# Performance work log

Hardware: AMD Instinct MI355X
Metric: run time of the kernel (lower is better)

Reference implementation:

```python
import jax, jax.numpy as jnp
import numpy as np

N = 100000
IN_C = 128
OUT_C = 32
HEADS = 4
E = 1600000
NEG_SLOPE = 0.2


def setup_inputs() -> dict:
    key = jax.random.key(0)
    ks = jax.random.split(key, 8)
    x = jax.random.normal(ks[0], (N, IN_C), dtype=jnp.float32)
    edge_index = jax.random.randint(ks[1], (2, E), 0, N, dtype=jnp.int64)
    # GATConv params (PyG conventions): lin weight [H*C, in], att vectors [H, C], bias [H*C]
    sc = 1.0 / np.sqrt(IN_C)
    W = jax.random.uniform(ks[2], (HEADS * OUT_C, IN_C), dtype=jnp.float32, minval=-sc, maxval=sc)
    att_src = jax.random.normal(ks[3], (HEADS, OUT_C), dtype=jnp.float32) * 0.1
    att_dst = jax.random.normal(ks[4], (HEADS, OUT_C), dtype=jnp.float32) * 0.1
    bias_conv = jnp.zeros((HEADS * OUT_C,), dtype=jnp.float32)
    # final nn.Linear(H*C, C)
    sl = 1.0 / np.sqrt(HEADS * OUT_C)
    W_lin = jax.random.uniform(ks[5], (OUT_C, HEADS * OUT_C), dtype=jnp.float32, minval=-sl, maxval=sl)
    b_lin = jax.random.uniform(ks[6], (OUT_C,), dtype=jnp.float32, minval=-sl, maxval=sl)
    return {"x": x, "edge_index": edge_index, "W": W, "att_src": att_src,
            "att_dst": att_dst, "bias_conv": bias_conv, "W_lin": W_lin, "b_lin": b_lin}


def reference(x, edge_index, W, att_src, att_dst, bias_conv, W_lin, b_lin):
    n = x.shape[0]
    # add self loops (PyG default)
    loops = jnp.arange(n, dtype=edge_index.dtype)
    src = jnp.concatenate([edge_index[0], loops])
    dst = jnp.concatenate([edge_index[1], loops])
    # linear projection, per-head split: [N, H, C]
    h = (x @ W.T).reshape(n, HEADS, OUT_C)
    # per-node attention logits
    a_src = jnp.einsum('nhc,hc->nh', h, att_src)  # [N, H]
    a_dst = jnp.einsum('nhc,hc->nh', h, att_dst)  # [N, H]
    e = a_src[src] + a_dst[dst]                   # [E', H]
    e = jax.nn.leaky_relu(e, NEG_SLOPE)
    # segment softmax over incoming edges per destination node
    m = jax.ops.segment_max(e, dst, num_segments=n)       # [N, H]
    e = jnp.exp(e - m[dst])
    s = jax.ops.segment_sum(e, dst, num_segments=n)       # [N, H]
    alpha = e / s[dst]                                    # [E', H]
    # scatter-aggregate alpha-weighted source features
    msg = alpha[:, :, None] * h[src]                      # [E', H, C]
    out = jax.ops.segment_sum(msg, dst, num_segments=n)   # [N, H, C]
    out = out.reshape(n, HEADS * OUT_C) + bias_conv
    # final linear + ELU
    return jax.nn.elu(out @ W_lin.T + b_lin)
```

## Files before the change

### kernel.cpp

```cpp
#include <hip/hip_runtime.h>
#include <hip/hip_fp16.h>
#include <cstdint>
#include <cstddef>

#define NHEADS 4
#define OUT_C 32
#define HC 128
#define IN_CH 128
#define NEG_SLOPE 0.2f
#define LDSPAD 136
#define KEDGE 4096

typedef _Float16 half8 __attribute__((ext_vector_type(8)));
typedef float floatx4 __attribute__((ext_vector_type(4)));

static inline size_t align256(size_t v) { return (v + 255) & ~(size_t)255; }

__device__ __forceinline__ float lrelu(float v) { return v > 0.f ? v : NEG_SLOPE * v; }

__device__ __forceinline__ float wred_sum(float v) {
    v += __shfl_xor(v, 1);
    v += __shfl_xor(v, 2);
    v += __shfl_xor(v, 4);
    v += __shfl_xor(v, 8);
    v += __shfl_xor(v, 16);
    v += __shfl_xor(v, 32);
    return v;
}

__device__ __forceinline__ unsigned int pack_h2(float a, float b) {
    __half2 h = __floats2half2_rn(a, b);
    return *reinterpret_cast<unsigned int*>(&h);
}
__device__ __forceinline__ float2 unpack_h2(unsigned int u) {
    __half2 h = *reinterpret_cast<__half2*>(&u);
    return __half22float2(h);
}

__global__ void dw(const float* __restrict__ W, _Float16* __restrict__ wh,
                   const int* __restrict__ ei, int* __restrict__ flag) {
    if (blockIdx.x < 64) {
        int idx = blockIdx.x * 256 + threadIdx.x;
        wh[idx] = (_Float16)W[idx];
        return;
    }
    __shared__ int red[256];
    int t = threadIdx.x;
    int acc = 0;
    for (int i = t; i < 1024; i += 256) acc |= ei[2 * i + 1];
    red[t] = acc;
    __syncthreads();
    for (int s = 128; s > 0; s >>= 1) {
        if (t < s) red[t] |= red[t + s];
        __syncthreads();
    }
    if (t == 0) *flag = (red[0] == 0) ? 1 : 0;
}

__global__ __launch_bounds__(256) void gemm_h(const float* __restrict__ x,
                                              const _Float16* __restrict__ wh,
                                              const float* __restrict__ att_src,
                                              const float* __restrict__ att_dst,
                                              __half* __restrict__ h,
                                              float* __restrict__ a_src,
                                              float* __restrict__ a_dst, int n) {
    __shared__ __align__(16) _Float16 Ws[128 * LDSPAD];
    __shared__ __align__(16) _Float16 Xs[128 * LDSPAD];
    int tid = threadIdx.x;
    int rowbase = blockIdx.x << 7;

    const uint4* w4 = (const uint4*)wh;
#pragma unroll
    for (int i = 0; i < 8; ++i) {
        int u = (i << 8) + tid;
        int r = u >> 4, g = u & 15;
        uint4 v = w4[u];
        *(uint4*)&Ws[r * LDSPAD + (g << 3)] = v;
    }
    const float4* x4 = (const float4*)x;
#pragma unroll
    for (int i = 0; i < 16; ++i) {
        int u = (i << 8) + tid;
        int r = u >> 5, c4 = u & 31;
        int row = rowbase + r;
        if (row >= n) row = n - 1;
        float4 v = x4[((size_t)row << 5) + c4];
        uint2 uu;
        uu.x = pack_h2(v.x, v.y);
        uu.y = pack_h2(v.z, v.w);
        *(uint2*)&Xs[r * LDSPAD + (c4 << 2)] = uu;
    }
    __syncthreads();

    int lane = tid & 63, w = tid >> 6;
    int quad = lane >> 4, Lm = lane & 15;
    floatx4 acc[2][8];
#pragma unroll
    for (int rt = 0; rt < 2; ++rt)
#pragma unroll
        for (int c = 0; c < 8; ++c) acc[rt][c] = (floatx4){0.f, 0.f, 0.f, 0.f};

#pragma unroll
    for (int kc = 0; kc < 128; kc += 32) {
        int ko = kc + (quad << 3);
        half8 a0 = *(const half8*)&Xs[((w << 5) + Lm) * LDSPAD + ko];
        half8 a1 = *(const half8*)&Xs[((w << 5) + 16 + Lm) * LDSPAD + ko];
#pragma unroll
        for (int c = 0; c < 8; ++c) {
            half8 b = *(const half8*)&Ws[((c << 4) + Lm) * LDSPAD + ko];
            acc[0][c] = __builtin_amdgcn_mfma_f32_16x16x32_f16(a0, b, acc[0][c], 0, 0, 0);
            acc[1][c] = __builtin_amdgcn_mfma_f32_16x16x32_f16(a1, b, acc[1][c], 0, 0, 0);
        }
    }
    __syncthreads();
#pragma unroll
    for (int rt = 0; rt < 2; ++rt)
#pragma unroll
        for (int c = 0; c < 8; ++c)
#pragma unroll
            for (int i = 0; i < 4; ++i) {
                int rl = (w << 5) + (rt << 4) + (quad << 2) + i;
                int cl = (c << 4) + Lm;
                Xs[rl * LDSPAD + cl] = (_Float16)acc[rt][c][i];
            }
    __syncthreads();
#pragma unroll
    for (int i = 0; i < 8; ++i) {
        int u = (i << 8) + tid;
        int r = u >> 4, g = u & 15;
        int row = rowbase + r;
        if (row < n) {
            uint4 v = *(uint4*)&Xs[r * LDSPAD + (g << 3)];
            *(uint4*)(h + ((size_t)row << 7) + (g << 3)) = v;
        }
    }
    int r = tid >> 1, seg = tid & 1;
    int row = rowbase + r;
    const _Float16* hp = &Xs[r * LDSPAD + (seg << 6)];
    float sa = 0.f, da = 0.f, sb = 0.f, db = 0.f;
#pragma unroll
    for (int g8 = 0; g8 < 8; ++g8) {
        half8 v = *(const half8*)&hp[g8 << 3];
        int co = (seg << 6) + (g8 << 3);
        float4 A1 = *(const float4*)&att_src[co];
        float4 A2 = *(const float4*)&att_src[co + 4];
        float4 D1 = *(const float4*)&att_dst[co];
        float4 D2 = *(const float4*)&att_dst[co + 4];
        float f0 = (float)v[0], f1 = (float)v[1], f2 = (float)v[2], f3 = (float)v[3];
        float f4 = (float)v[4], f5 = (float)v[5], f6 = (float)v[6], f7 = (float)v[7];
        float ts = f0 * A1.x + f1 * A1.y + f2 * A1.z + f3 * A1.w
                 + f4 * A2.x + f5 * A2.y + f6 * A2.z + f7 * A2.w;
        float td = f0 * D1.x + f1 * D1.y + f2 * D1.z + f3 * D1.w
                 + f4 * D2.x + f5 * D2.y + f6 * D2.z + f7 * D2.w;
        if (g8 < 4) { sa += ts; da += td; } else { sb += ts; db += td; }
    }
    if (row < n) {
        int base = (row << 2) + (seg << 1);
        a_src[base] = sa;
        a_src[base + 1] = sb;
        a_dst[base] = da;
        a_dst[base + 1] = db;
    }
}

__global__ void bhist(const int* __restrict__ ei, const int* __restrict__ flag,
                      int* __restrict__ bcount, int E, int sh) {
    __shared__ int c[256];
    int t = threadIdx.x;
    c[t] = 0;
    __syncthreads();
    int f64 = *flag;
    int stride = gridDim.x * 256;
    for (int i = blockIdx.x * 256 + t; i < E; i += stride) {
        int d;
        if (f64) d = (int)((const long long*)ei)[(size_t)E + i];
        else     d = ei[(size_t)E + i];
        atomicAdd(&c[d >> sh], 1);
    }
    __syncthreads();
    if (c[t]) atomicAdd(&bcount[t], c[t]);
}

__global__ void bscan(const int* __restrict__ bcount, int* __restrict__ bucket_base,
                      int* __restrict__ gcursor, int* __restrict__ off,
                      int n, int E, int sh) {
    __shared__ int ts[256];
    int t = threadIdx.x;
    int lo = t << sh, hi = (t + 1) << sh;
    if (hi > n) hi = n;
    int nodes = hi > lo ? hi - lo : 0;
    int v = bcount[t] + nodes;
    ts[t] = v;
    __syncthreads();
    int run = v;
    for (int d = 1; d < 256; d <<= 1) {
        int o = (t >= d) ? ts[t - d] : 0;
        __syncthreads();
        run += o;
        ts[t] = run;
        __syncthreads();
    }
    int excl = run - v;
    bucket_base[t] = excl;
    gcursor[t] = excl;
    if (t == 255) {
        bucket_base[256] = run;
        off[n] = E + n;
    }
}

__global__ __launch_bounds__(256) void bscatter(const int* __restrict__ ei,
                                                const int* __restrict__ flag,
                                                int* __restrict__ gcursor,
                                                int2* __restrict__ bkt,
                                                int E, int n, int sh) {
    __shared__ int cnt[256], base[256], lcur[256];
    int t = threadIdx.x;
    cnt[t] = 0;
    lcur[t] = 0;
    int total = E + n;
    int i0 = blockIdx.x * KEDGE;
    int f64 = *flag;
    int ed[16], es[16];
    __syncthreads();
#pragma unroll
    for (int j = 0; j < 16; ++j) {
        int i = i0 + (j << 8) + t;
        int s = 0, d = -1;
        if (i < total) {
            if (i < E) {
                if (f64) {
                    s = (int)((const long long*)ei)[i];
                    d = (int)((const long long*)ei)[(size_t)E + i];
                } else {
                    s = ei[i];
                    d = ei[(size_t)E + i];
                }
            } else {
                s = d = i - E;
            }
            atomicAdd(&cnt[d >> sh], 1);
        }
        ed[j] = d;
        es[j] = s;
    }
    __syncthreads();
    base[t] = cnt[t] ? atomicAdd(&gcursor[t], cnt[t]) : 0;
    __syncthreads();
#pragma unroll
    for (int j = 0; j < 16; ++j) {
        int d = ed[j];
        if (d >= 0) {
            int b = d >> sh;
            int pos = base[b] + atomicAdd(&lcur[b], 1);
            bkt[pos] = make_int2(d, es[j]);
        }
    }
}

__global__ __launch_bounds__(256) void bsort(const int2* __restrict__ bkt,
                                             const int* __restrict__ bucket_base,
                                             int* __restrict__ off,
                                             int* __restrict__ sorted,
                                             int n, int sh) {
    __shared__ int cnt[512], offl[512], ts[256];
    int t = threadIdx.x, bid = blockIdx.x;
    int node0 = bid << sh;
    int node1 = (bid + 1) << sh;
    if (node1 > n) node1 = n;
    int nn = node1 - node0;
    int e0 = bucket_base[bid], e1 = bucket_base[bid + 1];
    cnt[t] = 0;
    cnt[t + 256] = 0;
    __syncthreads();
    for (int i = e0 + t; i < e1; i += 256) {
        int2 e = bkt[i];
        atomicAdd(&cnt[e.x - node0], 1);
    }
    __syncthreads();
    int a = cnt[t << 1], b = cnt[(t << 1) + 1];
    int s = a + b;
    ts[t] = s;
    __syncthreads();
    int run = s;
    for (int d = 1; d < 256; d <<= 1) {
        int o = (t >= d) ? ts[t - d] : 0;
        __syncthreads();
        run += o;
        ts[t] = run;
        __syncthreads();
    }
    int excl = run - s;
    offl[t << 1] = excl;
    offl[(t << 1) + 1] = excl + a;
    cnt[t << 1] = 0;
    cnt[(t << 1) + 1] = 0;
    __syncthreads();
    for (int i = t; i < nn; i += 256) off[node0 + i] = e0 + offl[i];
    for (int i = e0 + t; i < e1; i += 256) {
        int2 e = bkt[i];
        int li = e.x - node0;
        int pos = e0 + offl[li] + atomicAdd(&cnt[li], 1);
        sorted[pos] = e.y;
    }
}

__device__ __forceinline__ void accum_half(const int* ssrc, const float* sal,
                                           const __half* __restrict__ h,
                                           int deg, int half, int L, int head,
                                           float4& acc) {
    float4 a0 = {0, 0, 0, 0}, a1 = {0, 0, 0, 0}, a2 = {0, 0, 0, 0}, a3 = {0, 0, 0, 0};
    int j = half;
    for (; j + 6 < deg; j += 8) {
        int s0 = ssrc[j], s1 = ssrc[j + 2], s2 = ssrc[j + 4], s3 = ssrc[j + 6];
        float w0 = sal[(j << 2) + head];
        float w1 = sal[((j + 2) << 2) + head];
        float w2 = sal[((j + 4) << 2) + head];
        float w3 = sal[((j + 6) << 2) + head];
        uint2 u0 = *(const uint2*)(h + ((size_t)s0 << 7) + (L << 2));
        uint2 u1 = *(const uint2*)(h + ((size_t)s1 << 7) + (L << 2));
        uint2 u2 = *(const uint2*)(h + ((size_t)s2 << 7) + (L << 2));
        uint2 u3 = *(const uint2*)(h + ((size_t)s3 << 7) + (L << 2));
        float2 f0a = unpack_h2(u0.x), f0b = unpack_h2(u0.y);
        float2 f1a = unpack_h2(u1.x), f1b = unpack_h2(u1.y);
        float2 f2a = unpack_h2(u2.x), f2b = unpack_h2(u2.y);
        float2 f3a = unpack_h2(u3.x), f3b = unpack_h2(u3.y);
        a0.x = fmaf(w0, f0a.x, a0.x); a0.y = fmaf(w0, f0a.y, a0.y);
        a0.z = fmaf(w0, f0b.x, a0.z); a0.w = fmaf(w0, f0b.y, a0.w);
        a1.x = fmaf(w1, f1a.x, a1.x); a1.y = fmaf(w1, f1a.y, a1.y);
        a1.z = fmaf(w1, f1b.x, a1.z); a1.w = fmaf(w1, f1b.y, a1.w);
        a2.x = fmaf(w2, f2a.x, a2.x); a2.y = fmaf(w2, f2a.y, a2.y);
        a2.z = fmaf(w2, f2b.x, a2.z); a2.w = fmaf(w2, f2b.y, a2.w);
        a3.x = fmaf(w3, f3a.x, a3.x); a3.y = fmaf(w3, f3a.y, a3.y);
        a3.z = fmaf(w3, f3b.x, a3.z); a3.w = fmaf(w3, f3b.y, a3.w);
    }
    for (; j < deg; j += 2) {
        int s0 = ssrc[j];
        float w0 = sal[(j << 2) + head];
        uint2 u0 = *(const uint2*)(h + ((size_t)s0 << 7) + (L << 2));
        float2 f0a = unpack_h2(u0.x), f0b = unpack_h2(u0.y);
        a0.x = fmaf(w0, f0a.x, a0.x); a0.y = fmaf(w0, f0a.y, a0.y);
        a0.z = fmaf(w0, f0b.x, a0.z); a0.w = fmaf(w0, f0b.y, a0.w);
    }
    acc.x += a0.x + a1.x + a2.x + a3.x;
    acc.y += a0.y + a1.y + a2.y + a3.y;
    acc.z += a0.z + a1.z + a2.z + a3.z;
    acc.w += a0.w + a1.w + a2.w + a3.w;
}

__global__ __launch_bounds__(256) void aggregate(const __half* __restrict__ h,
                                                 const int* __restrict__ sorted,
                                                 const int* __restrict__ off,
                                                 const float* __restrict__ a_src,
                                                 const float* __restrict__ a_dst,
                                                 const float* __restrict__ bias,
                                                 __half* __restrict__ agg, int n) {
    __shared__ __align__(16) int sh_src[4][64];
    __shared__ __align__(16) float sh_al[4][256];
    int wslot = threadIdx.x >> 6;
    int lane = threadIdx.x & 63;
    int wid = blockIdx.x * 4 + wslot;
    int nw = gridDim.x * 4;
    int L = lane & 31, half = lane >> 5, head = L >> 3;
    float4 b4 = ((const float4*)bias)[L];
    const float4* as4 = (const float4*)a_src;
    const float4* ad4 = (const float4*)a_dst;
    int* ssrc = sh_src[wslot];
    float* sal = sh_al[wslot];

    for (int node = wid; node < n; node += nw) {
        int start = off[node], end = off[node + 1];
        int deg = end - start;
        float4 ad = ad4[node];
        float4 acc = {0.f, 0.f, 0.f, 0.f};
        float4 psum = {0.f, 0.f, 0.f, 0.f};

        if (deg <= 64) {
            bool v = lane < deg;
            int idx = start + (v ? lane : 0);
            int s = sorted[idx];
            float4 as = as4[s];
            float4 p;
            p.x = v ? __expf(lrelu(as.x + ad.x)) : 0.f;
            p.y = v ? __expf(lrelu(as.y + ad.y)) : 0.f;
            p.z = v ? __expf(lrelu(as.z + ad.z)) : 0.f;
            p.w = v ? __expf(lrelu(as.w + ad.w)) : 0.f;
            psum = p;
            ssrc[lane] = s;
            *(float4*)&sal[lane << 2] = p;
            asm volatile("s_waitcnt lgkmcnt(0)" ::: "memory");
            accum_half(ssrc, sal, h, deg, half, L, head, acc);
            asm volatile("" ::: "memory");
        } else {
            for (int bb = 0; bb < deg; bb += 64) {
                int i = bb + lane;
                bool v = i < deg;
                int idx = start + (v ? i : 0);
                int s = sorted[idx];
                float4 as = as4[s];
                float4 p;
                p.x = v ? __expf(lrelu(as.x + ad.x)) : 0.f;
                p.y = v ? __expf(lrelu(as.y + ad.y)) : 0.f;
                p.z = v ? __expf(lrelu(as.z + ad.z)) : 0.f;
                p.w = v ? __expf(lrelu(as.w + ad.w)) : 0.f;
                psum.x += p.x; psum.y += p.y; psum.z += p.z; psum.w += p.w;
                ssrc[lane] = s;
                *(float4*)&sal[lane << 2] = p;
                asm volatile("s_waitcnt lgkmcnt(0)" ::: "memory");
                int cl = deg - bb;
                if (cl > 64) cl = 64;
                accum_half(ssrc, sal, h, cl, half, L, head, acc);
                asm volatile("" ::: "memory");
            }
        }
        float s0 = wred_sum(psum.x), s1 = wred_sum(psum.y);
        float s2 = wred_sum(psum.z), s3 = wred_sum(psum.w);
        float sh = (head == 0) ? s0 : (head == 1) ? s1 : (head == 2) ? s2 : s3;
        float inv = 1.f / sh;
        acc.x += __shfl_xor(acc.x, 32);
        acc.y += __shfl_xor(acc.y, 32);
        acc.z += __shfl_xor(acc.z, 32);
        acc.w += __shfl_xor(acc.w, 32);
        if (lane < 32) {
            float4 res = {fmaf(acc.x, inv, b4.x), fmaf(acc.y, inv, b4.y),
                          fmaf(acc.z, inv, b4.z), fmaf(acc.w, inv, b4.w)};
            uint2 u;
            u.x = pack_h2(res.x, res.y);
            u.y = pack_h2(res.z, res.w);
            *(uint2*)(agg + ((size_t)node << 7) + (L << 2)) = u;
        }
    }
}

__global__ __launch_bounds__(256) void proj(const __half* __restrict__ agg,
                                            const float* __restrict__ W_lin,
                                            const float* __restrict__ b_lin,
                                            float* __restrict__ out, int n) {
    __shared__ float xs[64][132];
    __shared__ float wt[128][36];
    int tid = threadIdx.x;
    const float4* w4 = (const float4*)W_lin;
#pragma unroll
    for (int i = 0; i < 4; ++i) {
        int f4 = (i << 8) + tid;
        int o = f4 >> 5, kk = (f4 & 31) << 2;
        float4 w = w4[f4];
        wt[kk][o] = w.x;
        wt[kk + 1][o] = w.y;
        wt[kk + 2][o] = w.z;
        wt[kk + 3][o] = w.w;
    }
    int rowbase = blockIdx.x << 6;
    const uint4* a4 = (const uint4*)agg;
#pragma unroll
    for (int i = 0; i < 4; ++i) {
        int f8 = (i << 8) + tid;
        int r = f8 >> 4, cc = (f8 & 15) << 3;
        int row = rowbase + r;
        if (row >= n) row = n - 1;
        uint4 u = a4[((size_t)row << 4) + (cc >> 3)];
        float2 f0 = unpack_h2(u.x), f1 = unpack_h2(u.y);
        float2 f2 = unpack_h2(u.z), f3 = unpack_h2(u.w);
        float* xp = &xs[r][cc];
        xp[0] = f0.x; xp[1] = f0.y; xp[2] = f1.x; xp[3] = f1.y;
        xp[4] = f2.x; xp[5] = f2.y; xp[6] = f3.x; xp[7] = f3.y;
    }
    __syncthreads();
    int r = tid >> 2, cg = tid & 3, c0 = cg << 3;
    float acc[8];
#pragma unroll
    for (int j = 0; j < 8; ++j) acc[j] = 0.f;
    for (int k = 0; k < 128; k += 4) {
        float4 xv = *(const float4*)&xs[r][k];
        float xk[4] = {xv.x, xv.y, xv.z, xv.w};
#pragma unroll
        for (int kk = 0; kk < 4; ++kk) {
            float4 wa = *(const float4*)&wt[k + kk][c0];
            float4 wb = *(const float4*)&wt[k + kk][c0 + 4];
            acc[0] = fmaf(xk[kk], wa.x, acc[0]);
            acc[1] = fmaf(xk[kk], wa.y, acc[1]);
            acc[2] = fmaf(xk[kk], wa.z, acc[2]);
            acc[3] = fmaf(xk[kk], wa.w, acc[3]);
            acc[4] = fmaf(xk[kk], wb.x, acc[4]);
            acc[5] = fmaf(xk[kk], wb.y, acc[5]);
            acc[6] = fmaf(xk[kk], wb.z, acc[6]);
            acc[7] = fmaf(xk[kk], wb.w, acc[7]);
        }
    }
    int row = rowbase + r;
    if (row < n) {
        float res[8];
#pragma unroll
        for (int j = 0; j < 8; ++j) {
            float v = acc[j] + b_lin[c0 + j];
            res[j] = v > 0.f ? v : (__expf(v) - 1.f);
        }
        float4* op = (float4*)(out + (size_t)row * 32 + c0);
        op[0] = make_float4(res[0], res[1], res[2], res[3]);
        op[1] = make_float4(res[4], res[5], res[6], res[7]);
    }
}

extern "C" void kernel_launch(void* const* d_in, const int* in_sizes, int n_in,
                              void* d_out, int out_size, void* d_ws, size_t ws_size,
                              hipStream_t stream) {
    const float* x = (const float*)d_in[0];
    const int* ei = (const int*)d_in[1];
    const float* W = (const float*)d_in[2];
    const float* att_src = (const float*)d_in[3];
    const float* att_dst = (const float*)d_in[4];
    const float* bias_conv = (const float*)d_in[5];
    const float* W_lin = (const float*)d_in[6];
    const float* b_lin = (const float*)d_in[7];
    int n = in_sizes[0] / IN_CH;
    int E = in_sizes[1] / 2;

    int sh = 0;
    while (((n + (1 << sh) - 1) >> sh) > 256) sh++;
    int NB = (n + (1 << sh) - 1) >> sh;

    char* ws = (char*)d_ws;
    size_t o = 0;
    auto alloc = [&](size_t bytes) { char* p = ws + o; o = align256(o + bytes); return p; };
    __half* h        = (__half*)alloc((size_t)n * HC * 2);
    __half* agg      = (__half*)alloc((size_t)n * HC * 2);
    _Float16* wh     = (_Float16*)alloc(128 * 128 * 2);
    float* a_src     = (float*)alloc((size_t)n * NHEADS * 4);
    float* a_dst     = (float*)alloc((size_t)n * NHEADS * 4);
    int* off         = (int*)alloc(((size_t)n + 1) * 4);
    int* bcount      = (int*)alloc(256 * 4);
    int* bucket_base = (int*)alloc(257 * 4);
    int* gcursor     = (int*)alloc(256 * 4);
    int* flag        = (int*)alloc(256);
    int* sorted      = (int*)alloc((size_t)(E + n + 64) * 4);
    int2* bkt        = (int2*)alloc((size_t)(E + n + 64) * 8);

    hipMemsetAsync(bcount, 0, 256 * 4, stream);

    dw<<<65, 256, 0, stream>>>(W, wh, ei, flag);
    gemm_h<<<(n + 127) / 128, 256, 0, stream>>>(x, wh, att_src, att_dst, h, a_src, a_dst, n);
    bhist<<<1024, 256, 0, stream>>>(ei, flag, bcount, E, sh);
    bscan<<<1, 256, 0, stream>>>(bcount, bucket_base, gcursor, off, n, E, sh);
    bscatter<<<(E + n + KEDGE - 1) / KEDGE, 256, 0, stream>>>(ei, flag, gcursor, bkt, E, n, sh);
    bsort<<<NB, 256, 0, stream>>>(bkt, bucket_base, off, sorted, n, sh);
    aggregate<<<2048, 256, 0, stream>>>(h, sorted, off, a_src, a_dst, bias_conv, agg, n);
    proj<<<(n + 63) / 64, 256, 0, stream>>>(agg, W_lin, b_lin, (float*)d_out, n);
}
```

Before: 309.6 us.

## Fold small setup kernels into consumers and deepen aggregate gather unroll

Removes the dw and bscan kernels. The fp32-to-fp16 weight conversion moves into gemm_h, the int64 detection is recomputed per block in bhist and bscatter, and the bucket prefix scan is redone redundantly in bscatter and bsort. gcursor now starts at zero, which relies on the memset covering bcount and gcursor together. The aggregate inner loop also gains a 16-edge unrolled stage to keep more gathers in flight. The aim is fewer launches and better memory-level parallelism, at the cost of redundant per-block scans and detection reads, and higher register pressure in aggregate.

```diff
diff --git a/kernel.cpp b/kernel.cpp
--- a/kernel.cpp
+++ b/kernel.cpp
@@ -37,28 +37,26 @@
     return __half22float2(h);
 }
 
-__global__ void dw(const float* __restrict__ W, _Float16* __restrict__ wh,
-                   const int* __restrict__ ei, int* __restrict__ flag) {
-    if (blockIdx.x < 64) {
-        int idx = blockIdx.x * 256 + threadIdx.x;
-        wh[idx] = (_Float16)W[idx];
-        return;
-    }
-    __shared__ int red[256];
+__device__ __forceinline__ int detect_f64(const int* __restrict__ ei, int E, int* sf) {
     int t = threadIdx.x;
+    if (t == 0) *sf = 0;
+    __syncthreads();
+    int lim = E < 1024 ? E : 1024;
     int acc = 0;
-    for (int i = t; i < 1024; i += 256) acc |= ei[2 * i + 1];
-    red[t] = acc;
-    __syncthreads();
-    for (int s = 128; s > 0; s >>= 1) {
-        if (t < s) red[t] |= red[t + s];
-        __syncthreads();
-    }
-    if (t == 0) *flag = (red[0] == 0) ? 1 : 0;
+    for (int i = t; i < lim; i += 256) acc |= ei[2 * i + 1];
+    acc |= __shfl_xor(acc, 1);
+    acc |= __shfl_xor(acc, 2);
+    acc |= __shfl_xor(acc, 4);
+    acc |= __shfl_xor(acc, 8);
+    acc |= __shfl_xor(acc, 16);
+    acc |= __shfl_xor(acc, 32);
+    if ((t & 63) == 0 && acc) atomicOr(sf, 1);
+    __syncthreads();
+    return *sf == 0;
 }
 
 __global__ __launch_bounds__(256) void gemm_h(const float* __restrict__ x,
-                                              const _Float16* __restrict__ wh,
+                                              const float* __restrict__ W,
                                               const float* __restrict__ att_src,
                                               const float* __restrict__ att_dst,
                                               __half* __restrict__ h,
@@ -69,13 +67,16 @@
     int tid = threadIdx.x;
     int rowbase = blockIdx.x << 7;
 
-    const uint4* w4 = (const uint4*)wh;
-#pragma unroll
-    for (int i = 0; i < 8; ++i) {
+    const float4* wf = (const float4*)W;
+#pragma unroll
+    for (int i = 0; i < 16; ++i) {
         int u = (i << 8) + tid;
-        int r = u >> 4, g = u & 15;
-        uint4 v = w4[u];
-        *(uint4*)&Ws[r * LDSPAD + (g << 3)] = v;
+        int r = u >> 5, g = u & 31;
+        float4 v = wf[u];
+        uint2 uu;
+        uu.x = pack_h2(v.x, v.y);
+        uu.y = pack_h2(v.z, v.w);
+        *(uint2*)&Ws[r * LDSPAD + (g << 2)] = uu;
     }
     const float4* x4 = (const float4*)x;
 #pragma unroll
@@ -163,13 +164,13 @@
     }
 }
 
-__global__ void bhist(const int* __restrict__ ei, const int* __restrict__ flag,
-                      int* __restrict__ bcount, int E, int sh) {
+__global__ void bhist(const int* __restrict__ ei, int* __restrict__ bcount,
+                      int E, int sh) {
     __shared__ int c[256];
+    __shared__ int sf;
     int t = threadIdx.x;
     c[t] = 0;
-    __syncthreads();
-    int f64 = *flag;
+    int f64 = detect_f64(ei, E, &sf);
     int stride = gridDim.x * 256;
     for (int i = blockIdx.x * 256 + t; i < E; i += stride) {
         int d;
@@ -181,48 +182,20 @@
     if (c[t]) atomicAdd(&bcount[t], c[t]);
 }
 
-__global__ void bscan(const int* __restrict__ bcount, int* __restrict__ bucket_base,
-                      int* __restrict__ gcursor, int* __restrict__ off,
-                      int n, int E, int sh) {
-    __shared__ int ts[256];
-    int t = threadIdx.x;
-    int lo = t << sh, hi = (t + 1) << sh;
-    if (hi > n) hi = n;
-    int nodes = hi > lo ? hi - lo : 0;
-    int v = bcount[t] + nodes;
-    ts[t] = v;
-    __syncthreads();
-    int run = v;
-    for (int d = 1; d < 256; d <<= 1) {
-        int o = (t >= d) ? ts[t - d] : 0;
-        __syncthreads();
-        run += o;
-        ts[t] = run;
-        __syncthreads();
-    }
-    int excl = run - v;
-    bucket_base[t] = excl;
-    gcursor[t] = excl;
-    if (t == 255) {
-        bucket_base[256] = run;
-        off[n] = E + n;
-    }
-}
-
 __global__ __launch_bounds__(256) void bscatter(const int* __restrict__ ei,
-                                                const int* __restrict__ flag,
+                                                const int* __restrict__ bcount,
                                                 int* __restrict__ gcursor,
                                                 int2* __restrict__ bkt,
                                                 int E, int n, int sh) {
-    __shared__ int cnt[256], base[256], lcur[256];
+    __shared__ int cnt[256], base[256], lcur[256], ts[256];
+    __shared__ int sf;
     int t = threadIdx.x;
     cnt[t] = 0;
     lcur[t] = 0;
+    int f64 = detect_f64(ei, E, &sf);
     int total = E + n;
     int i0 = blockIdx.x * KEDGE;
-    int f64 = *flag;
     int ed[16], es[16];
-    __syncthreads();
 #pragma unroll
     for (int j = 0; j < 16; ++j) {
         int i = i0 + (j << 8) + t;
@@ -244,8 +217,22 @@
         ed[j] = d;
         es[j] = s;
     }
-    __syncthreads();
-    base[t] = cnt[t] ? atomicAdd(&gcursor[t], cnt[t]) : 0;
+    int lo = t << sh, hi = (t + 1) << sh;
+    if (hi > n) hi = n;
+    int nodes = hi > lo ? hi - lo : 0;
+    int v = bcount[t] + nodes;
+    ts[t] = v;
+    __syncthreads();
+    int run = v;
+    for (int d = 1; d < 256; d <<= 1) {
+        int o = (t >= d) ? ts[t - d] : 0;
+        __syncthreads();
+        run += o;
+        ts[t] = run;
+        __syncthreads();
+    }
+    int excl = run - v;
+    base[t] = excl + (cnt[t] ? atomicAdd(&gcursor[t], cnt[t]) : 0);
     __syncthreads();
 #pragma unroll
     for (int j = 0; j < 16; ++j) {
@@ -259,30 +246,19 @@
 }
 
 __global__ __launch_bounds__(256) void bsort(const int2* __restrict__ bkt,
-                                             const int* __restrict__ bucket_base,
+                                             const int* __restrict__ bcount,
                                              int* __restrict__ off,
                                              int* __restrict__ sorted,
-                                             int n, int sh) {
+                                             int n, int E, int sh) {
     __shared__ int cnt[512], offl[512], ts[256];
     int t = threadIdx.x, bid = blockIdx.x;
-    int node0 = bid << sh;
-    int node1 = (bid + 1) << sh;
-    if (node1 > n) node1 = n;
-    int nn = node1 - node0;
-    int e0 = bucket_base[bid], e1 = bucket_base[bid + 1];
-    cnt[t] = 0;
-    cnt[t + 256] = 0;
-    __syncthreads();
-    for (int i = e0 + t; i < e1; i += 256) {
-        int2 e = bkt[i];
-        atomicAdd(&cnt[e.x - node0], 1);
-    }
-    __syncthreads();
-    int a = cnt[t << 1], b = cnt[(t << 1) + 1];
-    int s = a + b;
-    ts[t] = s;
-    __syncthreads();
-    int run = s;
+    int lo = t << sh, hi = (t + 1) << sh;
+    if (hi > n) hi = n;
+    int nodes = hi > lo ? hi - lo : 0;
+    int v = bcount[t] + nodes;
+    ts[t] = v;
+    __syncthreads();
+    int run = v;
     for (int d = 1; d < 256; d <<= 1) {
         int o = (t >= d) ? ts[t - d] : 0;
         __syncthreads();
@@ -290,6 +266,34 @@
         ts[t] = run;
         __syncthreads();
     }
+    int e0 = (bid > 0) ? ts[bid - 1] : 0;
+    int e1 = ts[bid];
+    if (bid == gridDim.x - 1 && t == 0) off[n] = E + n;
+    int node0 = bid << sh;
+    int node1 = (bid + 1) << sh;
+    if (node1 > n) node1 = n;
+    int nn = node1 - node0;
+    __syncthreads();
+    cnt[t] = 0;
+    cnt[t + 256] = 0;
+    __syncthreads();
+    for (int i = e0 + t; i < e1; i += 256) {
+        int2 e = bkt[i];
+        atomicAdd(&cnt[e.x - node0], 1);
+    }
+    __syncthreads();
+    int a = cnt[t << 1], b = cnt[(t << 1) + 1];
+    int s = a + b;
+    ts[t] = s;
+    __syncthreads();
+    run = s;
+    for (int d = 1; d < 256; d <<= 1) {
+        int o = (t >= d) ? ts[t - d] : 0;
+        __syncthreads();
+        run += o;
+        ts[t] = run;
+        __syncthreads();
+    }
     int excl = run - s;
     offl[t << 1] = excl;
     offl[(t << 1) + 1] = excl + a;
@@ -311,6 +315,51 @@
                                            float4& acc) {
     float4 a0 = {0, 0, 0, 0}, a1 = {0, 0, 0, 0}, a2 = {0, 0, 0, 0}, a3 = {0, 0, 0, 0};
     int j = half;
+    for (; j + 14 < deg; j += 16) {
+        int s0 = ssrc[j], s1 = ssrc[j + 2], s2 = ssrc[j + 4], s3 = ssrc[j + 6];
+        int s4 = ssrc[j + 8], s5 = ssrc[j + 10], s6 = ssrc[j + 12], s7 = ssrc[j + 14];
+        float w0 = sal[(j << 2) + head];
+        float w1 = sal[((j + 2) << 2) + head];
+        float w2 = sal[((j + 4) << 2) + head];
+        float w3 = sal[((j + 6) << 2) + head];
+        float w4 = sal[((j + 8) << 2) + head];
+        float w5 = sal[((j + 10) << 2) + head];
+        float w6 = sal[((j + 12) << 2) + head];
+        float w7 = sal[((j + 14) << 2) + head];
+        uint2 u0 = *(const uint2*)(h + ((size_t)s0 << 7) + (L << 2));
+        uint2 u1 = *(const uint2*)(h + ((size_t)s1 << 7) + (L << 2));
+        uint2 u2 = *(const uint2*)(h + ((size_t)s2 << 7) + (L << 2));
+        uint2 u3 = *(const uint2*)(h + ((size_t)s3 << 7) + (L << 2));
+        uint2 u4 = *(const uint2*)(h + ((size_t)s4 << 7) + (L << 2));
+        uint2 u5 = *(const uint2*)(h + ((size_t)s5 << 7) + (L << 2));
+        uint2 u6 = *(const uint2*)(h + ((size_t)s6 << 7) + (L << 2));
+        uint2 u7 = *(const uint2*)(h + ((size_t)s7 << 7) + (L << 2));
+        float2 fa, fb;
+        fa = unpack_h2(u0.x); fb = unpack_h2(u0.y);
+        a0.x = fmaf(w0, fa.x, a0.x); a0.y = fmaf(w0, fa.y, a0.y);
+        a0.z = fmaf(w0, fb.x, a0.z); a0.w = fmaf(w0, fb.y, a0.w);
+        fa = unpack_h2(u1.x); fb = unpack_h2(u1.y);
+        a1.x = fmaf(w1, fa.x, a1.x); a1.y = fmaf(w1, fa.y, a1.y);
+        a1.z = fmaf(w1, fb.x, a1.z); a1.w = fmaf(w1, fb.y, a1.w);
+        fa = unpack_h2(u2.x); fb = unpack_h2(u2.y);
+        a2.x = fmaf(w2, fa.x, a2.x); a2.y = fmaf(w2, fa.y, a2.y);
+        a2.z = fmaf(w2, fb.x, a2.z); a2.w = fmaf(w2, fb.y, a2.w);
+        fa = unpack_h2(u3.x); fb = unpack_h2(u3.y);
+        a3.x = fmaf(w3, fa.x, a3.x); a3.y = fmaf(w3, fa.y, a3.y);
+        a3.z = fmaf(w3, fb.x, a3.z); a3.w = fmaf(w3, fb.y, a3.w);
+        fa = unpack_h2(u4.x); fb = unpack_h2(u4.y);
+        a0.x = fmaf(w4, fa.x, a0.x); a0.y = fmaf(w4, fa.y, a0.y);
+        a0.z = fmaf(w4, fb.x, a0.z); a0.w = fmaf(w4, fb.y, a0.w);
+        fa = unpack_h2(u5.x); fb = unpack_h2(u5.y);
+        a1.x = fmaf(w5, fa.x, a1.x); a1.y = fmaf(w5, fa.y, a1.y);
+        a1.z = fmaf(w5, fb.x, a1.z); a1.w = fmaf(w5, fb.y, a1.w);
+        fa = unpack_h2(u6.x); fb = unpack_h2(u6.y);
+        a2.x = fmaf(w6, fa.x, a2.x); a2.y = fmaf(w6, fa.y, a2.y);
+        a2.z = fmaf(w6, fb.x, a2.z); a2.w = fmaf(w6, fb.y, a2.w);
+        fa = unpack_h2(u7.x); fb = unpack_h2(u7.y);
+        a3.x = fmaf(w7, fa.x, a3.x); a3.y = fmaf(w7, fa.y, a3.y);
+        a3.z = fmaf(w7, fb.x, a3.z); a3.w = fmaf(w7, fb.y, a3.w);
+    }
     for (; j + 6 < deg; j += 8) {
         int s0 = ssrc[j], s1 = ssrc[j + 2], s2 = ssrc[j + 4], s3 = ssrc[j + 6];
         float w0 = sal[(j << 2) + head];
@@ -321,31 +370,32 @@
         uint2 u1 = *(const uint2*)(h + ((size_t)s1 << 7) + (L << 2));
         uint2 u2 = *(const uint2*)(h + ((size_t)s2 << 7) + (L << 2));
         uint2 u3 = *(const uint2*)(h + ((size_t)s3 << 7) + (L << 2));
-        float2 f0a = unpack_h2(u0.x), f0b = unpack_h2(u0.y);
-        float2 f1a = unpack_h2(u1.x), f1b = unpack_h2(u1.y);
-        float2 f2a = unpack_h2(u2.x), f2b = unpack_h2(u2.y);
-        float2 f3a = unpack_h2(u3.x), f3b = unpack_h2(u3.y);
-        a0.x = fmaf(w0, f0a.x, a0.x); a0.y = fmaf(w0, f0a.y, a0.y);
-        a0.z = fmaf(w0, f0b.x, a0.z); a0.w = fmaf(w0, f0b.y, a0.w);
-        a1.x = fmaf(w1, f1a.x, a1.x); a1.y = fmaf(w1, f1a.y, a1.y);
-        a1.z = fmaf(w1, f1b.x, a1.z); a1.w = fmaf(w1, f1b.y, a1.w);
-        a2.x = fmaf(w2, f2a.x, a2.x); a2.y = fmaf(w2, f2a.y, a2.y);
-        a2.z = fmaf(w2, f2b.x, a2.z); a2.w = fmaf(w2, f2b.y, a2.w);
-        a3.x = fmaf(w3, f3a.x, a3.x); a3.y = fmaf(w3, f3a.y, a3.y);
-        a3.z = fmaf(w3, f3b.x, a3.z); a3.w = fmaf(w3, f3b.y, a3.w);
+        float2 fa, fb;
+        fa = unpack_h2(u0.x); fb = unpack_h2(u0.y);
+        a0.x = fmaf(w0, fa.x, a0.x); a0.y = fmaf(w0, fa.y, a0.y);
+        a0.z = fmaf(w0, fb.x, a0.z); a0.w = fmaf(w0, fb.y, a0.w);
+        fa = unpack_h2(u1.x); fb = unpack_h2(u1.y);
+        a1.x = fmaf(w1, fa.x, a1.x); a1.y = fmaf(w1, fa.y, a1.y);
+        a1.z = fmaf(w1, fb.x, a1.z); a1.w = fmaf(w1, fb.y, a1.w);
+        fa = unpack_h2(u2.x); fb = unpack_h2(u2.y);
+        a2.x = fmaf(w2, fa.x, a2.x); a2.y = fmaf(w2, fa.y, a2.y);
+        a2.z = fmaf(w2, fb.x, a2.z); a2.w = fmaf(w2, fb.y, a2.w);
+        fa = unpack_h2(u3.x); fb = unpack_h2(u3.y);
+        a3.x = fmaf(w3, fa.x, a3.x); a3.y = fmaf(w3, fa.y, a3.y);
+        a3.z = fmaf(w3, fb.x, a3.z); a3.w = fmaf(w3, fb.y, a3.w);
     }
     for (; j < deg; j += 2) {
         int s0 = ssrc[j];
         float w0 = sal[(j << 2) + head];
         uint2 u0 = *(const uint2*)(h + ((size_t)s0 << 7) + (L << 2));
-        float2 f0a = unpack_h2(u0.x), f0b = unpack_h2(u0.y);
-        a0.x = fmaf(w0, f0a.x, a0.x); a0.y = fmaf(w0, f0a.y, a0.y);
-        a0.z = fmaf(w0, f0b.x, a0.z); a0.w = fmaf(w0, f0b.y, a0.w);
-    }
-    acc.x += a0.x + a1.x + a2.x + a3.x;
-    acc.y += a0.y + a1.y + a2.y + a3.y;
-    acc.z += a0.z + a1.z + a2.z + a3.z;
-    acc.w += a0.w + a1.w + a2.w + a3.w;
+        float2 fa = unpack_h2(u0.x), fb = unpack_h2(u0.y);
+        a0.x = fmaf(w0, fa.x, a0.x); a0.y = fmaf(w0, fa.y, a0.y);
+        a0.z = fmaf(w0, fb.x, a0.z); a0.w = fmaf(w0, fb.y, a0.w);
+    }
+    acc.x += (a0.x + a1.x) + (a2.x + a3.x);
+    acc.y += (a0.y + a1.y) + (a2.y + a3.y);
+    acc.z += (a0.z + a1.z) + (a2.z + a3.z);
+    acc.w += (a0.w + a1.w) + (a2.w + a3.w);
 }
 
 __global__ __launch_bounds__(256) void aggregate(const __half* __restrict__ h,
@@ -522,27 +572,22 @@
     char* ws = (char*)d_ws;
     size_t o = 0;
     auto alloc = [&](size_t bytes) { char* p = ws + o; o = align256(o + bytes); return p; };
-    __half* h        = (__half*)alloc((size_t)n * HC * 2);
-    __half* agg      = (__half*)alloc((size_t)n * HC * 2);
-    _Float16* wh     = (_Float16*)alloc(128 * 128 * 2);
-    float* a_src     = (float*)alloc((size_t)n * NHEADS * 4);
-    float* a_dst     = (float*)alloc((size_t)n * NHEADS * 4);
-    int* off         = (int*)alloc(((size_t)n + 1) * 4);
-    int* bcount      = (int*)alloc(256 * 4);
-    int* bucket_base = (int*)alloc(257 * 4);
-    int* gcursor     = (int*)alloc(256 * 4);
-    int* flag        = (int*)alloc(256);
-    int* sorted      = (int*)alloc((size_t)(E + n + 64) * 4);
-    int2* bkt        = (int2*)alloc((size_t)(E + n + 64) * 8);
-
-    hipMemsetAsync(bcount, 0, 256 * 4, stream);
-
-    dw<<<65, 256, 0, stream>>>(W, wh, ei, flag);
-    gemm_h<<<(n + 127) / 128, 256, 0, stream>>>(x, wh, att_src, att_dst, h, a_src, a_dst, n);
-    bhist<<<1024, 256, 0, stream>>>(ei, flag, bcount, E, sh);
-    bscan<<<1, 256, 0, stream>>>(bcount, bucket_base, gcursor, off, n, E, sh);
-    bscatter<<<(E + n + KEDGE - 1) / KEDGE, 256, 0, stream>>>(ei, flag, gcursor, bkt, E, n, sh);
-    bsort<<<NB, 256, 0, stream>>>(bkt, bucket_base, off, sorted, n, sh);
+    __half* h      = (__half*)alloc((size_t)n * HC * 2);
+    __half* agg    = (__half*)alloc((size_t)n * HC * 2);
+    float* a_src   = (float*)alloc((size_t)n * NHEADS * 4);
+    float* a_dst   = (float*)alloc((size_t)n * NHEADS * 4);
+    int* off       = (int*)alloc(((size_t)n + 1) * 4);
+    int* bcount    = (int*)alloc(256 * 4);
+    int* gcursor   = (int*)alloc(256 * 4);
+    int* sorted    = (int*)alloc((size_t)(E + n + 64) * 4);
+    int2* bkt      = (int2*)alloc((size_t)(E + n + 64) * 8);
+
+    hipMemsetAsync(bcount, 0, 2048, stream);
+
+    gemm_h<<<(n + 127) / 128, 256, 0, stream>>>(x, W, att_src, att_dst, h, a_src, a_dst, n);
+    bhist<<<1024, 256, 0, stream>>>(ei, bcount, E, sh);
+    bscatter<<<(E + n + KEDGE - 1) / KEDGE, 256, 0, stream>>>(ei, bcount, gcursor, bkt, E, n, sh);
+    bsort<<<NB, 256, 0, stream>>>(bkt, bcount, off, sorted, n, E, sh);
     aggregate<<<2048, 256, 0, stream>>>(h, sorted, off, a_src, a_dst, bias_conv, agg, n);
     proj<<<(n + 63) / 64, 256, 0, stream>>>(agg, W_lin, b_lin, (float*)d_out, n);
 }
```

Result: faster. 303.3 us (-2.0%).
